# Kernel tuning notes

Hardware: AMD Instinct MI355X
Metric: run time of the kernel (lower is better)

Reference implementation:

```python
import jax, jax.numpy as jnp
import numpy as np

B, S, F, H, C, L = 256, 128, 128, 512, 64, 16


def setup_inputs() -> dict:
    key = jax.random.key(0)
    ks = jax.random.split(key, 16)
    stdv = 1.0 / np.sqrt(H)
    u = lambda k, shape, s=stdv: jax.random.uniform(k, shape, jnp.float32, -s, s)
    W_ih = u(ks[0], (F, 4 * H))
    b_ih = u(ks[1], (4 * H,)).at[H:2 * H].set(1.0)  # forget-gate bias init = 1
    W_hh = u(ks[2], (H, 4 * H))
    b_hh = u(ks[3], (4 * H,)).at[H:2 * H].set(1.0)
    cg_w1 = u(ks[4], (C, H))
    cg_b1 = u(ks[5], (H,))
    cg_w2 = u(ks[6], (H, 3 * H))
    cg_b2 = jnp.ones((3 * H,), jnp.float32)  # context_gate[-2].bias.fill_(1.0)
    mu_w = u(ks[7], (H, L))
    mu_b = u(ks[8], (L,))
    lv_w = u(ks[9], (H, L))
    lv_b = u(ks[10], (L,))
    dec_w1 = u(ks[11], (L, H))
    dec_b1 = u(ks[12], (H,))
    dec_w2 = u(ks[13], (H, F))
    dec_b2 = u(ks[14], (F,))
    kx, kc, ke = jax.random.split(ks[15], 3)
    return dict(
        x=jax.random.normal(kx, (B, S, F), jnp.float32),
        context=jax.random.normal(kc, (B, C), jnp.float32),
        eps=jax.random.normal(ke, (B, L), jnp.float32),
        W_ih=W_ih, b_ih=b_ih, W_hh=W_hh, b_hh=b_hh,
        cg_w1=cg_w1, cg_b1=cg_b1, cg_w2=cg_w2, cg_b2=cg_b2,
        mu_w=mu_w, mu_b=mu_b, lv_w=lv_w, lv_b=lv_b,
        dec_w1=dec_w1, dec_b1=dec_b1, dec_w2=dec_w2, dec_b2=dec_b2,
    )


def reference(x, context, eps, W_ih, b_ih, W_hh, b_hh, cg_w1, cg_b1, cg_w2, cg_b2,
              mu_w, mu_b, lv_w, lv_b, dec_w1, dec_b1, dec_w2, dec_b2):
    Bsz, Slen, _ = x.shape
    Hd = W_hh.shape[0]
    # context is static across time -> context-gate computed once (same math as
    # recomputing identically at each step)
    ctx = jax.nn.sigmoid(jax.nn.relu(context @ cg_w1 + cg_b1) @ cg_w2 + cg_b2)  # [B, 3H]
    ci, cf, co = jnp.split(ctx, 3, axis=1)
    # precompute input projections for all timesteps: [S, B, 4H]
    xg = jnp.einsum('bsf,fk->sbk', x, W_ih) + b_ih

    def step(carry, xg_t):
        h, c = carry
        gates = xg_t + h @ W_hh + b_hh
        i, f, g, o = jnp.split(gates, 4, axis=1)
        i = jax.nn.sigmoid(i) * ci
        f = jax.nn.sigmoid(f) * cf
        g = jnp.tanh(g)
        o = jax.nn.sigmoid(o) * co
        c_next = f * c + i * g
        h_next = o * jnp.tanh(c_next)
        return (h_next, c_next), None

    h0 = jnp.zeros((Bsz, Hd), x.dtype)
    (h, _), _ = jax.lax.scan(step, (h0, h0), xg)

    mu = h @ mu_w + mu_b
    log_var = h @ lv_w + lv_b
    z = mu + eps * jnp.exp(0.5 * log_var)  # reparameterize
    recon_x = jax.nn.relu(z @ dec_w1 + dec_b1) @ dec_w2 + dec_b2
    return recon_x, mu, log_var
```

## Files before the change

kernel.cpp:

```cpp
#include <hip/hip_runtime.h>
#include <cstdint>
#include <cstddef>

#define B_ 256
#define S_ 128
#define F_ 128
#define H_ 512
#define C_ 64
#define L_ 16

typedef __attribute__((ext_vector_type(8))) short short8;
typedef __attribute__((ext_vector_type(4))) float f4;
typedef __attribute__((ext_vector_type(4))) unsigned int u4;

__device__ __forceinline__ unsigned short f2bf(float f) {
  union { float f; unsigned u; } v; v.f = f;
  unsigned r = v.u + 0x7fffu + ((v.u >> 16) & 1u);
  return (unsigned short)(r >> 16);
}
__device__ __forceinline__ float sigmoid_(float x) { return 1.0f / (1.0f + __expf(-x)); }
__device__ __forceinline__ float tanh_(float x) {
  x = fminf(15.f, fmaxf(-15.f, x));
  float e = __expf(2.f * x);
  return (e - 1.f) / (e + 1.f);
}

__global__ void prepack_w(const float* __restrict__ W_hh, const float* __restrict__ W_ih,
                          const float* __restrict__ b_ih, const float* __restrict__ b_hh,
                          unsigned short* __restrict__ Wpk, unsigned short* __restrict__ Wipk,
                          float* __restrict__ bc) {
  int t = blockIdx.x * blockDim.x + threadIdx.x;
  if (t < 131072) {
    int lane = t & 63, row = t >> 6;
    int kit = row & 15, gh = row >> 4;
    int g = gh & 3, ht = gh >> 2;
    int k0 = kit * 32 + ((lane >> 4) << 3);
    int col = g * 512 + ht * 16 + (lane & 15);
#pragma unroll
    for (int j = 0; j < 8; j++)
      Wpk[t * 8 + j] = f2bf(W_hh[(k0 + j) * 2048 + col]);
  } else if (t < 131072 + 32768) {
    int t2 = t - 131072;
    int lane = t2 & 63, row = t2 >> 6;
    int kit = row & 3, gh = row >> 2;
    int g = gh & 3, ht = gh >> 2;
    int k0 = kit * 32 + ((lane >> 4) << 3);
    int col = g * 512 + ht * 16 + (lane & 15);
#pragma unroll
    for (int j = 0; j < 8; j++)
      Wipk[t2 * 8 + j] = f2bf(W_ih[(k0 + j) * 2048 + col]);
  } else if (t < 131072 + 32768 + 2048) {
    int i = t - 131072 - 32768;
    bc[i] = b_ih[i] + b_hh[i];
  }
}

__global__ void prepack_x(const float* __restrict__ x, unsigned short* __restrict__ xfr) {
  int o8 = blockIdx.x * blockDim.x + threadIdx.x;
  int m = o8 & 15, kb = (o8 >> 4) & 15, Rg = (o8 >> 8) & 15, s = o8 >> 12;
  int b = Rg * 16 + m;
  const float* src = x + (b * S_ + s) * F_ + kb * 8;
  unsigned short* dst = xfr + o8 * 8;
#pragma unroll
  for (int j = 0; j < 8; j++) dst[j] = f2bf(src[j]);
}

__global__ void ctx1_kernel(const float* __restrict__ context, const float* __restrict__ w1,
                            const float* __restrict__ b1, float* __restrict__ hid1) {
  __shared__ float cc[C_];
  int b = blockIdx.x, t = threadIdx.x;
  if (t < C_) cc[t] = context[b * C_ + t];
  __syncthreads();
  for (int j = t; j < H_; j += 256) {
    float acc = b1[j];
#pragma unroll 8
    for (int k = 0; k < C_; k++) acc = fmaf(cc[k], w1[k * H_ + j], acc);
    hid1[b * H_ + j] = fmaxf(acc, 0.f);
  }
}

__global__ void ctx2_kernel(const float* __restrict__ hid1, const float* __restrict__ w2,
                            const float* __restrict__ b2, float* __restrict__ ctxg) {
  __shared__ float hr[4 * H_];
  int r0 = blockIdx.x * 4, t = threadIdx.x;
  for (int i = t; i < 4 * H_; i += 256) hr[i] = hid1[r0 * H_ + i];
  __syncthreads();
  float acc[4][6];
#pragma unroll
  for (int r = 0; r < 4; r++)
#pragma unroll
    for (int i = 0; i < 6; i++) acc[r][i] = 0.f;
  for (int k = 0; k < H_; k++) {
    float w[6];
#pragma unroll
    for (int i = 0; i < 6; i++) w[i] = w2[k * 1536 + t + i * 256];
#pragma unroll
    for (int r = 0; r < 4; r++) {
      float hv = hr[r * H_ + k];
#pragma unroll
      for (int i = 0; i < 6; i++) acc[r][i] = fmaf(hv, w[i], acc[r][i]);
    }
  }
#pragma unroll
  for (int r = 0; r < 4; r++)
#pragma unroll
    for (int i = 0; i < 6; i++) {
      int col = t + i * 256;
      ctxg[(r0 + r) * 1536 + col] = sigmoid_(acc[r][i] + b2[col]);
    }
}

__global__ void __launch_bounds__(256) lstm_kernel(
    const unsigned short* __restrict__ xfr, const unsigned short* __restrict__ Wpk,
    const unsigned short* __restrict__ Wipk, const float* __restrict__ bc,
    const float* __restrict__ ctxg, float* __restrict__ hfinal,
    unsigned short* __restrict__ hb0, unsigned short* __restrict__ hb1,
    unsigned int* __restrict__ ctr) {
  __shared__ __align__(16) unsigned short lds_h[16384];
  __shared__ __align__(16) unsigned short lds_x[4096];
  __shared__ float lds_g[128 * 17];

  int tid = threadIdx.x, lane = tid & 63, wid = tid >> 6;
  int bt = blockIdx.x >> 5, ht = blockIdx.x & 31;

  short8 wf[16], wfi[4];
  {
    const short8* wp = (const short8*)Wpk + (ht * 4 + wid) * 16 * 64 + lane;
#pragma unroll
    for (int kit = 0; kit < 16; kit++) wf[kit] = wp[kit * 64];
    const short8* wip = (const short8*)Wipk + (ht * 4 + wid) * 4 * 64 + lane;
#pragma unroll
    for (int kit = 0; kit < 4; kit++) wfi[kit] = wip[kit * 64];
  }

  int bl = tid >> 3, jl0 = (tid & 7) * 2;
  int bglob = bt * 32 + bl;
  int j0 = ht * 16 + jl0;
  float cst[2] = {0.f, 0.f};
  float ci_[2], cf_[2], co_[2], bi_[2], bf_[2], bg_[2], bo_[2];
#pragma unroll
  for (int p = 0; p < 2; p++) {
    int j = j0 + p;
    ci_[p] = ctxg[bglob * 1536 + j];
    cf_[p] = ctxg[bglob * 1536 + 512 + j];
    co_[p] = ctxg[bglob * 1536 + 1024 + j];
    bi_[p] = bc[j]; bf_[p] = bc[512 + j]; bg_[p] = bc[1024 + j]; bo_[p] = bc[1536 + j];
  }
  int hoff2 = (((bt * 2 + (bl >> 4)) * 64 + ht * 2 + (jl0 >> 3)) * 128
               + (bl & 15) * 8 + (jl0 & 7)) >> 1;

#pragma unroll
  for (int i = 0; i < 2; i++) {
    int c = wid * 2 + i, R = c >> 2, kit = c & 3;
    u4 d = *(const u4*)(xfr + (size_t)((bt * 2 + R) * 16 + kit * 4) * 128 + lane * 8);
    *(u4*)(lds_x + (R * 4 + kit) * 512 + lane * 8) = d;
  }
  __syncthreads();

  for (int t = 0; t < S_; t++) {
    const unsigned short* hread = (t & 1) ? hb1 : hb0;
    unsigned short* hwrite = (t & 1) ? hb0 : hb1;

    if (t > 0) {
      const unsigned int* cb = ctr + (unsigned)((t - 1) * 8 + bt) * 256;
      for (;;) {
        unsigned a = __hip_atomic_load(cb,       __ATOMIC_RELAXED, __HIP_MEMORY_SCOPE_AGENT);
        unsigned b = __hip_atomic_load(cb + 64,  __ATOMIC_RELAXED, __HIP_MEMORY_SCOPE_AGENT);
        unsigned c = __hip_atomic_load(cb + 128, __ATOMIC_RELAXED, __HIP_MEMORY_SCOPE_AGENT);
        unsigned d = __hip_atomic_load(cb + 192, __ATOMIC_RELAXED, __HIP_MEMORY_SCOPE_AGENT);
        if (a + b + c + d >= 128u) break;
      }
    }

    u4 tmp[8];
#pragma unroll
    for (int i = 0; i < 8; i++) {
      int c = wid * 8 + i, R = c >> 4, kit = c & 15;
      const unsigned int* src = (const unsigned int*)hread
          + (bt * 2 + R) * 4096 + kit * 256 + lane * 4;
      asm volatile("global_load_dwordx4 %0, %1, off sc0 sc1"
                   : "=v"(tmp[i]) : "v"(src) : "memory");
    }

    f4 acc0 = {0.f, 0.f, 0.f, 0.f}, acc1 = {0.f, 0.f, 0.f, 0.f};
#pragma unroll
    for (int kit = 0; kit < 4; kit++) {
      short8 a0 = *(const short8*)(lds_x + kit * 512 + lane * 8);
      short8 a1 = *(const short8*)(lds_x + 2048 + kit * 512 + lane * 8);
      acc0 = __builtin_amdgcn_mfma_f32_16x16x32_bf16(a0, wfi[kit], acc0, 0, 0, 0);
      acc1 = __builtin_amdgcn_mfma_f32_16x16x32_bf16(a1, wfi[kit], acc1, 0, 0, 0);
    }

    asm volatile("s_waitcnt vmcnt(0)"
                 : "+v"(tmp[0]), "+v"(tmp[1]), "+v"(tmp[2]), "+v"(tmp[3]),
                   "+v"(tmp[4]), "+v"(tmp[5]), "+v"(tmp[6]), "+v"(tmp[7])
                 :: "memory");
#pragma unroll
    for (int i = 0; i < 8; i++) {
      int c = wid * 8 + i, R = c >> 4, kit = c & 15;
      *(u4*)(lds_h + R * 8192 + kit * 512 + lane * 8) = tmp[i];
    }
    __syncthreads();

#pragma unroll
    for (int kit = 0; kit < 16; kit++) {
      short8 a0 = *(const short8*)(lds_h + kit * 512 + lane * 8);
      short8 a1 = *(const short8*)(lds_h + 8192 + kit * 512 + lane * 8);
      acc0 = __builtin_amdgcn_mfma_f32_16x16x32_bf16(a0, wf[kit], acc0, 0, 0, 0);
      acc1 = __builtin_amdgcn_mfma_f32_16x16x32_bf16(a1, wf[kit], acc1, 0, 0, 0);
    }

    {
      int q = lane >> 4, n = lane & 15;
#pragma unroll
      for (int r = 0; r < 4; r++) {
        lds_g[(wid * 32 + q * 4 + r) * 17 + n] = acc0[r];
        lds_g[(wid * 32 + 16 + q * 4 + r) * 17 + n] = acc1[r];
      }
    }
    __syncthreads();

    {
      float hv[2];
#pragma unroll
      for (int p = 0; p < 2; p++) {
        int jl = jl0 + p;
        float gi = lds_g[(0 * 32 + bl) * 17 + jl] + bi_[p];
        float gf = lds_g[(1 * 32 + bl) * 17 + jl] + bf_[p];
        float gg = lds_g[(2 * 32 + bl) * 17 + jl] + bg_[p];
        float go = lds_g[(3 * 32 + bl) * 17 + jl] + bo_[p];
        float iv = ci_[p] * sigmoid_(gi);
        float fv = cf_[p] * sigmoid_(gf);
        float ov = co_[p] * sigmoid_(go);
        float gv = tanh_(gg);
        float c = fv * cst[p] + iv * gv;
        cst[p] = c;
        hv[p] = ov * tanh_(c);
      }
      unsigned int packed = (unsigned)f2bf(hv[0]) | ((unsigned)f2bf(hv[1]) << 16);
      unsigned int* dst = (unsigned int*)hwrite + hoff2;
      asm volatile("global_store_dword %0, %1, off sc0 sc1"
                   :: "v"(dst), "v"(packed) : "memory");
      if (t == S_ - 1) {
        hfinal[bglob * H_ + j0] = hv[0];
        hfinal[bglob * H_ + j0 + 1] = hv[1];
      }
    }

    if (t < S_ - 1) {
      asm volatile("s_waitcnt vmcnt(0)" ::: "memory");
      if (lane == 0)
        __hip_atomic_fetch_add(ctr + (unsigned)(t * 8 + bt) * 256 + wid * 64, 1u,
                               __ATOMIC_RELAXED, __HIP_MEMORY_SCOPE_AGENT);
#pragma unroll
      for (int i = 0; i < 2; i++) {
        int c = wid * 2 + i, R = c >> 2, kit = c & 3;
        u4 d = *(const u4*)(xfr + (size_t)((((t + 1) * 16) + bt * 2 + R) * 16 + kit * 4) * 128 + lane * 8);
        *(u4*)(lds_x + (R * 4 + kit) * 512 + lane * 8) = d;
      }
    }
    __syncthreads();
  }
}

__global__ void post_kernel(const float* __restrict__ hfinal, const float* __restrict__ eps,
                            const float* __restrict__ mu_w, const float* __restrict__ mu_b,
                            const float* __restrict__ lv_w, const float* __restrict__ lv_b,
                            const float* __restrict__ dw1, const float* __restrict__ db1,
                            const float* __restrict__ dw2, const float* __restrict__ db2,
                            float* __restrict__ out) {
  __shared__ float sh[H_], sh1[H_], smu[L_], slv[L_], sz[L_];
  int b = blockIdx.x, t = threadIdx.x;
  for (int i = t; i < H_; i += 256) sh[i] = hfinal[b * H_ + i];
  __syncthreads();
  {
    int o = t >> 3, sub = t & 7, l = o & 15;
    const float* w = (o < 16) ? mu_w : lv_w;
    float acc = 0.f;
    int k0 = sub * 64;
#pragma unroll 8
    for (int k = k0; k < k0 + 64; k++) acc = fmaf(sh[k], w[k * L_ + l], acc);
#pragma unroll
    for (int d = 4; d >= 1; d >>= 1) acc += __shfl_down(acc, d, 8);
    if (sub == 0) {
      if (o < 16) { float v = acc + mu_b[l]; smu[l] = v; out[32768 + b * 16 + l] = v; }
      else        { float v = acc + lv_b[l]; slv[l] = v; out[36864 + b * 16 + l] = v; }
    }
  }
  __syncthreads();
  if (t < L_) sz[t] = smu[t] + eps[b * L_ + t] * __expf(0.5f * slv[t]);
  __syncthreads();
  for (int j = t; j < H_; j += 256) {
    float acc = db1[j];
#pragma unroll
    for (int l = 0; l < L_; l++) acc = fmaf(sz[l], dw1[l * H_ + j], acc);
    sh1[j] = fmaxf(acc, 0.f);
  }
  __syncthreads();
  if (t < F_) {
    float acc = db2[t];
    for (int k = 0; k < H_; k++) acc = fmaf(sh1[k], dw2[k * F_ + t], acc);
    out[b * F_ + t] = acc;
  }
}

extern "C" void kernel_launch(void* const* d_in, const int* in_sizes, int n_in,
                              void* d_out, int out_size, void* d_ws, size_t ws_size,
                              hipStream_t stream) {
  const float* x      = (const float*)d_in[0];
  const float* ctxin  = (const float*)d_in[1];
  const float* eps    = (const float*)d_in[2];
  const float* W_ih   = (const float*)d_in[3];
  const float* b_ih   = (const float*)d_in[4];
  const float* W_hh   = (const float*)d_in[5];
  const float* b_hh   = (const float*)d_in[6];
  const float* cg_w1  = (const float*)d_in[7];
  const float* cg_b1  = (const float*)d_in[8];
  const float* cg_w2  = (const float*)d_in[9];
  const float* cg_b2  = (const float*)d_in[10];
  const float* mu_w   = (const float*)d_in[11];
  const float* mu_b   = (const float*)d_in[12];
  const float* lv_w   = (const float*)d_in[13];
  const float* lv_b   = (const float*)d_in[14];
  const float* dec_w1 = (const float*)d_in[15];
  const float* dec_b1 = (const float*)d_in[16];
  const float* dec_w2 = (const float*)d_in[17];
  const float* dec_b2 = (const float*)d_in[18];
  float* out = (float*)d_out;

  char* ws = (char*)d_ws;
  size_t off = 0;
  auto alloc = [&](size_t bytes) { char* p = ws + off; off = (off + bytes + 255) & ~(size_t)255; return p; };

  unsigned short* hb0 = (unsigned short*)alloc(B_ * H_ * 2);
  unsigned short* hb1 = (unsigned short*)alloc(B_ * H_ * 2);
  unsigned int*   ctr = (unsigned int*)alloc(128 * 8 * 256 * 4);
  size_t zero_bytes = off;
  unsigned short* xfr  = (unsigned short*)alloc((size_t)B_ * S_ * F_ * 2);
  unsigned short* Wpk  = (unsigned short*)alloc((size_t)H_ * 2048 * 2);
  unsigned short* Wipk = (unsigned short*)alloc((size_t)F_ * 2048 * 2);
  float* bc    = (float*)alloc(2048 * 4);
  float* ctxg  = (float*)alloc((size_t)B_ * 1536 * 4);
  float* hid1  = (float*)alloc((size_t)B_ * H_ * 4);
  float* hfin  = (float*)alloc((size_t)B_ * H_ * 4);
  (void)ws_size; (void)in_sizes; (void)n_in; (void)out_size;

  hipMemsetAsync(d_ws, 0, zero_bytes, stream);

  prepack_w<<<648, 256, 0, stream>>>(W_hh, W_ih, b_ih, b_hh, Wpk, Wipk, bc);
  prepack_x<<<2048, 256, 0, stream>>>(x, xfr);
  ctx1_kernel<<<256, 256, 0, stream>>>(ctxin, cg_w1, cg_b1, hid1);
  ctx2_kernel<<<64, 256, 0, stream>>>(hid1, cg_w2, cg_b2, ctxg);
  lstm_kernel<<<256, 256, 0, stream>>>(xfr, Wpk, Wipk, bc, ctxg, hfin, hb0, hb1, ctr);
  post_kernel<<<256, 256, 0, stream>>>(hfin, eps, mu_w, mu_b, lv_w, lv_b,
                                       dec_w1, dec_b1, dec_w2, dec_b2, out);
}
```

Before: 569.8 us.

## Replace per-step atomic counters with monotonic flags and fuse prep kernels

Inter-block synchronisation in the LSTM recurrence switches from per-timestep atomic-add counters to one monotonically increasing flag per block. Each wave polls all 32 flags of its batch tile in parallel with a wave vote. The input-projection MFMAs are issued before the wait, the recurrent GEMM is skipped at t=0, and split accumulators add MFMA ILP. The four preprocessing kernels are fused into one launch with the context MLP kept in shared memory, removing launches, the hid1 buffer and a large memset. This relies on flag-ordering correctness through the block barrier and coherent stores.

```diff
diff --git a/kernel.cpp b/kernel.cpp
--- a/kernel.cpp
+++ b/kernel.cpp
@@ -25,89 +25,90 @@
   return (e - 1.f) / (e + 1.f);
 }
 
-__global__ void prepack_w(const float* __restrict__ W_hh, const float* __restrict__ W_ih,
-                          const float* __restrict__ b_ih, const float* __restrict__ b_hh,
-                          unsigned short* __restrict__ Wpk, unsigned short* __restrict__ Wipk,
-                          float* __restrict__ bc) {
-  int t = blockIdx.x * blockDim.x + threadIdx.x;
-  if (t < 131072) {
-    int lane = t & 63, row = t >> 6;
-    int kit = row & 15, gh = row >> 4;
-    int g = gh & 3, ht = gh >> 2;
-    int k0 = kit * 32 + ((lane >> 4) << 3);
-    int col = g * 512 + ht * 16 + (lane & 15);
-#pragma unroll
-    for (int j = 0; j < 8; j++)
-      Wpk[t * 8 + j] = f2bf(W_hh[(k0 + j) * 2048 + col]);
-  } else if (t < 131072 + 32768) {
-    int t2 = t - 131072;
-    int lane = t2 & 63, row = t2 >> 6;
-    int kit = row & 3, gh = row >> 2;
-    int g = gh & 3, ht = gh >> 2;
-    int k0 = kit * 32 + ((lane >> 4) << 3);
-    int col = g * 512 + ht * 16 + (lane & 15);
-#pragma unroll
-    for (int j = 0; j < 8; j++)
-      Wipk[t2 * 8 + j] = f2bf(W_ih[(k0 + j) * 2048 + col]);
-  } else if (t < 131072 + 32768 + 2048) {
-    int i = t - 131072 - 32768;
-    bc[i] = b_ih[i] + b_hh[i];
-  }
-}
-
-__global__ void prepack_x(const float* __restrict__ x, unsigned short* __restrict__ xfr) {
-  int o8 = blockIdx.x * blockDim.x + threadIdx.x;
-  int m = o8 & 15, kb = (o8 >> 4) & 15, Rg = (o8 >> 8) & 15, s = o8 >> 12;
-  int b = Rg * 16 + m;
-  const float* src = x + (b * S_ + s) * F_ + kb * 8;
-  unsigned short* dst = xfr + o8 * 8;
-#pragma unroll
-  for (int j = 0; j < 8; j++) dst[j] = f2bf(src[j]);
-}
-
-__global__ void ctx1_kernel(const float* __restrict__ context, const float* __restrict__ w1,
-                            const float* __restrict__ b1, float* __restrict__ hid1) {
-  __shared__ float cc[C_];
-  int b = blockIdx.x, t = threadIdx.x;
-  if (t < C_) cc[t] = context[b * C_ + t];
-  __syncthreads();
-  for (int j = t; j < H_; j += 256) {
-    float acc = b1[j];
+__global__ void prep_kernel(const float* __restrict__ x, const float* __restrict__ W_hh,
+                            const float* __restrict__ W_ih, const float* __restrict__ b_ih,
+                            const float* __restrict__ b_hh, const float* __restrict__ context,
+                            const float* __restrict__ w1, const float* __restrict__ b1,
+                            const float* __restrict__ w2, const float* __restrict__ b2,
+                            unsigned short* __restrict__ xfr, unsigned short* __restrict__ Wpk,
+                            unsigned short* __restrict__ Wipk, float* __restrict__ bc,
+                            float* __restrict__ ctxg) {
+  int bid = blockIdx.x, tid = threadIdx.x;
+  if (bid < 2048) {
+    int o8 = bid * 256 + tid;
+    int m = o8 & 15, kb = (o8 >> 4) & 15, Rg = (o8 >> 8) & 15, s = o8 >> 12;
+    int b = Rg * 16 + m;
+    const float* src = x + (b * S_ + s) * F_ + kb * 8;
+    unsigned short* dst = xfr + o8 * 8;
+#pragma unroll
+    for (int j = 0; j < 8; j++) dst[j] = f2bf(src[j]);
+    return;
+  }
+  if (bid < 2696) {
+    int t = (bid - 2048) * 256 + tid;
+    if (t < 131072) {
+      int lane = t & 63, row = t >> 6;
+      int kit = row & 15, gh = row >> 4;
+      int g = gh & 3, ht = gh >> 2;
+      int k0 = kit * 32 + ((lane >> 4) << 3);
+      int col = g * 512 + ht * 16 + (lane & 15);
+#pragma unroll
+      for (int j = 0; j < 8; j++)
+        Wpk[t * 8 + j] = f2bf(W_hh[(k0 + j) * 2048 + col]);
+    } else if (t < 131072 + 32768) {
+      int t2 = t - 131072;
+      int lane = t2 & 63, row = t2 >> 6;
+      int kit = row & 3, gh = row >> 2;
+      int g = gh & 3, ht = gh >> 2;
+      int k0 = kit * 32 + ((lane >> 4) << 3);
+      int col = g * 512 + ht * 16 + (lane & 15);
+#pragma unroll
+      for (int j = 0; j < 8; j++)
+        Wipk[t2 * 8 + j] = f2bf(W_ih[(k0 + j) * 2048 + col]);
+    } else if (t < 131072 + 32768 + 2048) {
+      int i = t - 131072 - 32768;
+      bc[i] = b_ih[i] + b_hh[i];
+    }
+    return;
+  }
+  {
+    __shared__ float hr[4 * H_];
+    __shared__ float cc[4 * C_];
+    int r0 = (bid - 2696) * 4, t = tid;
+    if (t < 4 * C_) cc[t] = context[r0 * C_ + t];
+    __syncthreads();
+    for (int rj = t; rj < 4 * H_; rj += 256) {
+      int r = rj >> 9, j = rj & 511;
+      float acc = b1[j];
 #pragma unroll 8
-    for (int k = 0; k < C_; k++) acc = fmaf(cc[k], w1[k * H_ + j], acc);
-    hid1[b * H_ + j] = fmaxf(acc, 0.f);
-  }
-}
-
-__global__ void ctx2_kernel(const float* __restrict__ hid1, const float* __restrict__ w2,
-                            const float* __restrict__ b2, float* __restrict__ ctxg) {
-  __shared__ float hr[4 * H_];
-  int r0 = blockIdx.x * 4, t = threadIdx.x;
-  for (int i = t; i < 4 * H_; i += 256) hr[i] = hid1[r0 * H_ + i];
-  __syncthreads();
-  float acc[4][6];
-#pragma unroll
-  for (int r = 0; r < 4; r++)
-#pragma unroll
-    for (int i = 0; i < 6; i++) acc[r][i] = 0.f;
-  for (int k = 0; k < H_; k++) {
-    float w[6];
-#pragma unroll
-    for (int i = 0; i < 6; i++) w[i] = w2[k * 1536 + t + i * 256];
-#pragma unroll
-    for (int r = 0; r < 4; r++) {
-      float hv = hr[r * H_ + k];
-#pragma unroll
-      for (int i = 0; i < 6; i++) acc[r][i] = fmaf(hv, w[i], acc[r][i]);
-    }
-  }
-#pragma unroll
-  for (int r = 0; r < 4; r++)
-#pragma unroll
-    for (int i = 0; i < 6; i++) {
-      int col = t + i * 256;
-      ctxg[(r0 + r) * 1536 + col] = sigmoid_(acc[r][i] + b2[col]);
-    }
+      for (int k = 0; k < C_; k++) acc = fmaf(cc[r * C_ + k], w1[k * H_ + j], acc);
+      hr[rj] = fmaxf(acc, 0.f);
+    }
+    __syncthreads();
+    float acc[4][6];
+#pragma unroll
+    for (int r = 0; r < 4; r++)
+#pragma unroll
+      for (int i = 0; i < 6; i++) acc[r][i] = 0.f;
+    for (int k = 0; k < H_; k++) {
+      float w[6];
+#pragma unroll
+      for (int i = 0; i < 6; i++) w[i] = w2[k * 1536 + t + i * 256];
+#pragma unroll
+      for (int r = 0; r < 4; r++) {
+        float hv = hr[r * H_ + k];
+#pragma unroll
+        for (int i = 0; i < 6; i++) acc[r][i] = fmaf(hv, w[i], acc[r][i]);
+      }
+    }
+#pragma unroll
+    for (int r = 0; r < 4; r++)
+#pragma unroll
+      for (int i = 0; i < 6; i++) {
+        int col = t + i * 256;
+        ctxg[(r0 + r) * 1536 + col] = sigmoid_(acc[r][i] + b2[col]);
+      }
+  }
 }
 
 __global__ void __launch_bounds__(256) lstm_kernel(
@@ -115,7 +116,7 @@
     const unsigned short* __restrict__ Wipk, const float* __restrict__ bc,
     const float* __restrict__ ctxg, float* __restrict__ hfinal,
     unsigned short* __restrict__ hb0, unsigned short* __restrict__ hb1,
-    unsigned int* __restrict__ ctr) {
+    unsigned int* __restrict__ flags) {
   __shared__ __align__(16) unsigned short lds_h[16384];
   __shared__ __align__(16) unsigned short lds_x[4096];
   __shared__ float lds_g[128 * 17];
@@ -149,6 +150,9 @@
   int hoff2 = (((bt * 2 + (bl >> 4)) * 64 + ht * 2 + (jl0 >> 3)) * 128
                + (bl & 15) * 8 + (jl0 & 7)) >> 1;
 
+  const unsigned int* fb = flags + bt * 32;
+  unsigned int* myflag = flags + bt * 32 + ht;
+
 #pragma unroll
   for (int i = 0; i < 2; i++) {
     int c = wid * 2 + i, R = c >> 2, kit = c & 3;
@@ -161,61 +165,74 @@
     const unsigned short* hread = (t & 1) ? hb1 : hb0;
     unsigned short* hwrite = (t & 1) ? hb0 : hb1;
 
-    if (t > 0) {
-      const unsigned int* cb = ctr + (unsigned)((t - 1) * 8 + bt) * 256;
-      for (;;) {
-        unsigned a = __hip_atomic_load(cb,       __ATOMIC_RELAXED, __HIP_MEMORY_SCOPE_AGENT);
-        unsigned b = __hip_atomic_load(cb + 64,  __ATOMIC_RELAXED, __HIP_MEMORY_SCOPE_AGENT);
-        unsigned c = __hip_atomic_load(cb + 128, __ATOMIC_RELAXED, __HIP_MEMORY_SCOPE_AGENT);
-        unsigned d = __hip_atomic_load(cb + 192, __ATOMIC_RELAXED, __HIP_MEMORY_SCOPE_AGENT);
-        if (a + b + c + d >= 128u) break;
-      }
-    }
-
-    u4 tmp[8];
-#pragma unroll
-    for (int i = 0; i < 8; i++) {
-      int c = wid * 8 + i, R = c >> 4, kit = c & 15;
-      const unsigned int* src = (const unsigned int*)hread
-          + (bt * 2 + R) * 4096 + kit * 256 + lane * 4;
-      asm volatile("global_load_dwordx4 %0, %1, off sc0 sc1"
-                   : "=v"(tmp[i]) : "v"(src) : "memory");
-    }
-
-    f4 acc0 = {0.f, 0.f, 0.f, 0.f}, acc1 = {0.f, 0.f, 0.f, 0.f};
+    f4 acc0a = {0.f, 0.f, 0.f, 0.f}, acc1a = {0.f, 0.f, 0.f, 0.f};
+    f4 acc0b = {0.f, 0.f, 0.f, 0.f}, acc1b = {0.f, 0.f, 0.f, 0.f};
+
 #pragma unroll
     for (int kit = 0; kit < 4; kit++) {
       short8 a0 = *(const short8*)(lds_x + kit * 512 + lane * 8);
       short8 a1 = *(const short8*)(lds_x + 2048 + kit * 512 + lane * 8);
-      acc0 = __builtin_amdgcn_mfma_f32_16x16x32_bf16(a0, wfi[kit], acc0, 0, 0, 0);
-      acc1 = __builtin_amdgcn_mfma_f32_16x16x32_bf16(a1, wfi[kit], acc1, 0, 0, 0);
-    }
-
-    asm volatile("s_waitcnt vmcnt(0)"
-                 : "+v"(tmp[0]), "+v"(tmp[1]), "+v"(tmp[2]), "+v"(tmp[3]),
-                   "+v"(tmp[4]), "+v"(tmp[5]), "+v"(tmp[6]), "+v"(tmp[7])
-                 :: "memory");
-#pragma unroll
-    for (int i = 0; i < 8; i++) {
-      int c = wid * 8 + i, R = c >> 4, kit = c & 15;
-      *(u4*)(lds_h + R * 8192 + kit * 512 + lane * 8) = tmp[i];
-    }
-    __syncthreads();
-
-#pragma unroll
-    for (int kit = 0; kit < 16; kit++) {
-      short8 a0 = *(const short8*)(lds_h + kit * 512 + lane * 8);
-      short8 a1 = *(const short8*)(lds_h + 8192 + kit * 512 + lane * 8);
-      acc0 = __builtin_amdgcn_mfma_f32_16x16x32_bf16(a0, wf[kit], acc0, 0, 0, 0);
-      acc1 = __builtin_amdgcn_mfma_f32_16x16x32_bf16(a1, wf[kit], acc1, 0, 0, 0);
+      if (kit & 1) {
+        acc0b = __builtin_amdgcn_mfma_f32_16x16x32_bf16(a0, wfi[kit], acc0b, 0, 0, 0);
+        acc1b = __builtin_amdgcn_mfma_f32_16x16x32_bf16(a1, wfi[kit], acc1b, 0, 0, 0);
+      } else {
+        acc0a = __builtin_amdgcn_mfma_f32_16x16x32_bf16(a0, wfi[kit], acc0a, 0, 0, 0);
+        acc1a = __builtin_amdgcn_mfma_f32_16x16x32_bf16(a1, wfi[kit], acc1a, 0, 0, 0);
+      }
+    }
+
+    if (t > 0) {
+      const unsigned int* fp = fb + (lane & 31);
+      unsigned tgt = (unsigned)t;
+      for (;;) {
+        unsigned v = __hip_atomic_load(fp, __ATOMIC_RELAXED, __HIP_MEMORY_SCOPE_AGENT);
+        if (__all(v >= tgt)) break;
+      }
+
+      u4 tmp[8];
+#pragma unroll
+      for (int i = 0; i < 8; i++) {
+        int c = wid * 8 + i, R = c >> 4, kit = c & 15;
+        const unsigned int* src = (const unsigned int*)hread
+            + (bt * 2 + R) * 4096 + kit * 256 + lane * 4;
+        asm volatile("global_load_dwordx4 %0, %1, off sc0 sc1"
+                     : "=v"(tmp[i]) : "v"(src) : "memory");
+      }
+
+      asm volatile("s_waitcnt vmcnt(0)"
+                   : "+v"(tmp[0]), "+v"(tmp[1]), "+v"(tmp[2]), "+v"(tmp[3]),
+                     "+v"(tmp[4]), "+v"(tmp[5]), "+v"(tmp[6]), "+v"(tmp[7])
+                   :: "memory");
+#pragma unroll
+      for (int i = 0; i < 8; i++) {
+        int c = wid * 8 + i, R = c >> 4, kit = c & 15;
+        *(u4*)(lds_h + R * 8192 + kit * 512 + lane * 8) = tmp[i];
+      }
+      __syncthreads();
+
+#pragma unroll
+      for (int kit = 0; kit < 16; kit++) {
+        short8 a0 = *(const short8*)(lds_h + kit * 512 + lane * 8);
+        short8 a1 = *(const short8*)(lds_h + 8192 + kit * 512 + lane * 8);
+        if (kit & 1) {
+          acc0b = __builtin_amdgcn_mfma_f32_16x16x32_bf16(a0, wf[kit], acc0b, 0, 0, 0);
+          acc1b = __builtin_amdgcn_mfma_f32_16x16x32_bf16(a1, wf[kit], acc1b, 0, 0, 0);
+        } else {
+          acc0a = __builtin_amdgcn_mfma_f32_16x16x32_bf16(a0, wf[kit], acc0a, 0, 0, 0);
+          acc1a = __builtin_amdgcn_mfma_f32_16x16x32_bf16(a1, wf[kit], acc1a, 0, 0, 0);
+        }
+      }
     }
 
     {
+      f4 s0, s1;
+#pragma unroll
+      for (int r = 0; r < 4; r++) { s0[r] = acc0a[r] + acc0b[r]; s1[r] = acc1a[r] + acc1b[r]; }
       int q = lane >> 4, n = lane & 15;
 #pragma unroll
       for (int r = 0; r < 4; r++) {
-        lds_g[(wid * 32 + q * 4 + r) * 17 + n] = acc0[r];
-        lds_g[(wid * 32 + 16 + q * 4 + r) * 17 + n] = acc1[r];
+        lds_g[(wid * 32 + q * 4 + r) * 17 + n] = s0[r];
+        lds_g[(wid * 32 + 16 + q * 4 + r) * 17 + n] = s1[r];
       }
     }
     __syncthreads();
@@ -249,9 +266,12 @@
 
     if (t < S_ - 1) {
       asm volatile("s_waitcnt vmcnt(0)" ::: "memory");
-      if (lane == 0)
-        __hip_atomic_fetch_add(ctr + (unsigned)(t * 8 + bt) * 256 + wid * 64, 1u,
-                               __ATOMIC_RELAXED, __HIP_MEMORY_SCOPE_AGENT);
+      __syncthreads();
+      if (tid == 0) {
+        unsigned val = (unsigned)(t + 1);
+        asm volatile("global_store_dword %0, %1, off sc0 sc1"
+                     :: "v"(myflag), "v"(val) : "memory");
+      }
 #pragma unroll
       for (int i = 0; i < 2; i++) {
         int c = wid * 2 + i, R = c >> 2, kit = c & 3;
@@ -332,26 +352,25 @@
   size_t off = 0;
   auto alloc = [&](size_t bytes) { char* p = ws + off; off = (off + bytes + 255) & ~(size_t)255; return p; };
 
+  unsigned int* flags = (unsigned int*)alloc(8 * 32 * 4);
+  size_t zero_bytes = off;
   unsigned short* hb0 = (unsigned short*)alloc(B_ * H_ * 2);
   unsigned short* hb1 = (unsigned short*)alloc(B_ * H_ * 2);
-  unsigned int*   ctr = (unsigned int*)alloc(128 * 8 * 256 * 4);
-  size_t zero_bytes = off;
   unsigned short* xfr  = (unsigned short*)alloc((size_t)B_ * S_ * F_ * 2);
   unsigned short* Wpk  = (unsigned short*)alloc((size_t)H_ * 2048 * 2);
   unsigned short* Wipk = (unsigned short*)alloc((size_t)F_ * 2048 * 2);
   float* bc    = (float*)alloc(2048 * 4);
   float* ctxg  = (float*)alloc((size_t)B_ * 1536 * 4);
-  float* hid1  = (float*)alloc((size_t)B_ * H_ * 4);
   float* hfin  = (float*)alloc((size_t)B_ * H_ * 4);
   (void)ws_size; (void)in_sizes; (void)n_in; (void)out_size;
 
   hipMemsetAsync(d_ws, 0, zero_bytes, stream);
 
-  prepack_w<<<648, 256, 0, stream>>>(W_hh, W_ih, b_ih, b_hh, Wpk, Wipk, bc);
-  prepack_x<<<2048, 256, 0, stream>>>(x, xfr);
-  ctx1_kernel<<<256, 256, 0, stream>>>(ctxin, cg_w1, cg_b1, hid1);
-  ctx2_kernel<<<64, 256, 0, stream>>>(hid1, cg_w2, cg_b2, ctxg);
-  lstm_kernel<<<256, 256, 0, stream>>>(xfr, Wpk, Wipk, bc, ctxg, hfin, hb0, hb1, ctr);
+  prep_kernel<<<2760, 256, 0, stream>>>(x, W_hh, W_ih, b_ih, b_hh, ctxin,
+                                        cg_w1, cg_b1, cg_w2, cg_b2,
+                                        xfr, Wpk, Wipk, bc, ctxg);
+  lstm_kernel<<<256, 256, 0, stream>>>(xfr, Wpk, Wipk, bc, ctxg, hfin, hb0, hb1,
+                                       flags);
   post_kernel<<<256, 256, 0, stream>>>(hfin, eps, mu_w, mu_b, lv_w, lv_b,
                                        dec_w1, dec_b1, dec_w2, dec_b2, out);
 }
```

Result: slower. 610.7 us (+7.2%).
